# Optimization experiments

Measured on AMD Instinct MI355X. Metric: run time of the kernel, lower is better.

The kernel has to match this reference:

```python
import jax, jax.numpy as jnp
import numpy as np

B, T, H, W, C = 2, 8, 20, 36, 512
NH = 4
HD = C // NH
WS = (5, 9)
EXP = (2, 4)              # window_size // 2
KP = (5, 9)               # focal unfold kernel for level k=0
PADP = (2, 4)
T2T_K, T2T_S, T2T_P = (7, 7), (3, 3), (3, 3)
FFN_HD = 1960
NWH, NWW = H // WS[0], W // WS[1]   # 4, 4
WAREA = WS[0] * WS[1]               # 45


def _valid_ind_rolled():
    wh, ww = WS
    eh, ew = EXP
    m = np.ones((4, wh, ww), np.float32)
    m[0, :wh - eh, :ww - ew] = 0   # tl
    m[1, :wh - eh, ew:] = 0        # tr
    m[2, eh:, :ww - ew] = 0        # bl
    m[3, eh:, ew:] = 0             # br
    return jnp.asarray(np.nonzero(m.reshape(-1))[0])

VALID_ROLLED = _valid_ind_rolled()  # (120,)


def unfold(x, k, s, p):
    # x: (N, Cc, Hh, Ww) -> (N, Cc*kh*kw, L); matches torch.nn.Unfold layout (c slowest).
    N, Cc, Hh, Ww = x.shape
    kh, kw = k; sh, sw = s; ph, pw = p
    xp = jnp.pad(x, ((0, 0), (0, 0), (ph, ph), (pw, pw)))
    oh = (Hh + 2 * ph - kh) // sh + 1
    ow = (Ww + 2 * pw - kw) // sw + 1
    cols = [xp[:, :, i:i + oh * sh:sh, j:j + ow * sw:sw]
            for i in range(kh) for j in range(kw)]
    patches = jnp.stack(cols, axis=2)            # (N, Cc, kh*kw, oh, ow)
    return patches.reshape(N, Cc * kh * kw, oh * ow)


def fold(patches, out_hw, k, s, p):
    # inverse of unfold (overlap-add), matches torch F.fold.
    N = patches.shape[0]
    kh, kw = k; sh, sw = s; ph, pw = p
    Hh, Ww = out_hw
    oh = (Hh + 2 * ph - kh) // sh + 1
    ow = (Ww + 2 * pw - kw) // sw + 1
    Cc = patches.shape[1] // (kh * kw)
    pr = patches.reshape(N, Cc, kh, kw, oh, ow)
    out = jnp.zeros((N, Cc, Hh + 2 * ph, Ww + 2 * pw), patches.dtype)
    for i in range(kh):
        for j in range(kw):
            out = out.at[:, :, i:i + oh * sh:sh, j:j + ow * sw:sw].add(pr[:, :, i, j])
    return out[:, :, ph:ph + Hh, pw:pw + Ww]


def layer_norm(x, g, b):
    mu = jnp.mean(x, -1, keepdims=True)
    var = jnp.var(x, -1, keepdims=True)
    return (x - mu) * jax.lax.rsqrt(var + 1e-5) * g + b


def win_part(x):
    # (B,T,H,W,C) -> (B*nW, T*wh*ww, C)
    b = x.shape[0]
    x = x.reshape(b, T, NWH, WS[0], NWW, WS[1], C)
    return x.transpose(0, 2, 4, 1, 3, 5, 6).reshape(-1, T * WAREA, C)


def to_heads(w):
    return w.reshape(-1, T, WAREA, NH, HD).transpose(0, 3, 1, 2, 4).reshape(-1, NH, T * WAREA, HD)


def block_forward(x, g1, be1, wqkv, bqkv, wproj, bproj, wpool, bpool, g2, be2, w1, bf1, w2, bf2, out_h, out_w):
    shortcut = x
    xn = layer_norm(x, g1, be1)

    # ---- coarser (pooled) focal level, k=0 (focal_level=2) ----
    wnr = xn.reshape(B, T, NWH, WS[0], NWW, WS[1], C).transpose(0, 2, 4, 1, 3, 5, 6)
    wnr = wnr.reshape(B, NWH, NWW, T, WAREA, C)
    pooled = jnp.einsum('bhwtnc,n->bhwtc', wnr, wpool) + bpool   # (B,NWH,NWW,T,C)

    # ---- window attention ----
    qkv = xn @ wqkv + bqkv                                       # (B,T,H,W,3C)
    q, k, v = jnp.split(qkv, 3, axis=-1)
    qw = to_heads(win_part(q)) * (HD ** -0.5)
    kw_, vw = to_heads(win_part(k)), to_heads(win_part(v))

    def rolled(t):
        parts = []
        for sh, sw in ((-EXP[0], -EXP[1]), (-EXP[0], EXP[1]), (EXP[0], -EXP[1]), (EXP[0], EXP[1])):
            r = jnp.roll(t, (sh, sw), axis=(2, 3))
            parts.append(win_part(r).reshape(-1, T, WAREA, NH, HD))
        cat = jnp.concatenate(parts, axis=2)                     # (B*nW, T, 4*warea, NH, HD)
        cat = jnp.take(cat.transpose(0, 3, 1, 2, 4), VALID_ROLLED, axis=3)
        return cat.reshape(-1, NH, T * VALID_ROLLED.shape[0], HD)

    k_rolled = jnp.concatenate([kw_, rolled(k)], axis=2)         # (B*nW, NH, T*165, HD)
    v_rolled = jnp.concatenate([vw, rolled(v)], axis=2)

    # pooled keys/values via focal unfold
    xp = pooled.transpose(0, 3, 1, 2, 4)                          # (B,T,NWH,NWW,C)
    qkv_p = xp @ wqkv + bqkv
    kp, vp = qkv_p[..., C:2 * C], qkv_p[..., 2 * C:]

    def unfold_kv(t):
        t = t.transpose(0, 1, 4, 2, 3).reshape(B * T, C, NWH, NWW)
        u = unfold(t, KP, (1, 1), PADP)                           # (B*T, C*45, L)
        L = u.shape[-1]
        u = u.reshape(B, T, C, KP[0], KP[1], L).transpose(0, 5, 1, 3, 4, 2)
        u = u.reshape(B * L, T, KP[0] * KP[1], NH, HD).transpose(0, 3, 1, 2, 4)
        return u.reshape(B * L, NH, T * KP[0] * KP[1], HD)

    k_all = jnp.concatenate([k_rolled, unfold_kv(kp)], axis=2)
    v_all = jnp.concatenate([v_rolled, unfold_kv(vp)], axis=2)

    attn = jnp.einsum('wnqd,wnkd->wnqk', qw, k_all)               # (B*nW, NH, T*45, N)

    # validity mask for pooled context (zero-padded unfold positions -> -100)
    ones = jnp.ones((T, 1, NWH, NWW), x.dtype)
    um = unfold(ones, KP, (1, 1), PADP)                           # (T, 45, L)
    L = um.shape[-1]
    mvals = jnp.where(um.reshape(T, KP[0] * KP[1], L).transpose(2, 0, 1).reshape(L, -1) == 0,
                      jnp.asarray(-100.0, x.dtype), jnp.asarray(0.0, x.dtype))
    n_rolled = k_rolled.shape[2]
    mask_cols = jnp.concatenate([jnp.zeros((L, n_rolled), x.dtype), mvals], axis=1)
    attn = attn + jnp.tile(mask_cols, (B, 1))[:, None, None, :]

    attn = jax.nn.softmax(attn, axis=-1)
    out = jnp.einsum('wnqk,wnkd->wnqd', attn, v_all)
    out = out.transpose(0, 2, 1, 3).reshape(-1, T * WAREA, C) @ wproj + bproj

    # window reverse + residual
    out = out.reshape(B, NWH, NWW, T, WS[0], WS[1], C)
    out = out.transpose(0, 3, 1, 4, 2, 5, 6).reshape(B, T, H, W, C)
    x = shortcut + out

    # ---- FusionFeedForward (fold/unfold re-normalized MLP) ----
    y = layer_norm(x, g2, be2).reshape(B, T * H * W, C)
    h = y @ w1 + bf1                                              # (B, n, 1960)
    nvec = ((out_h + 2 * T2T_P[0] - T2T_K[0]) // T2T_S[0] + 1) * \
           ((out_w + 2 * T2T_P[1] - T2T_K[1]) // T2T_S[1] + 1)
    bt = (B * T * H * W) // nvec
    norm_p = jnp.ones((bt, T2T_K[0] * T2T_K[1], nvec), x.dtype)
    norm_f = fold(norm_p, (out_h, out_w), T2T_K, T2T_S, T2T_P)    # (bt,1,out_h,out_w)
    h_f = fold(h.reshape(bt, nvec, FFN_HD).transpose(0, 2, 1), (out_h, out_w), T2T_K, T2T_S, T2T_P)
    h = unfold(h_f / norm_f, T2T_K, T2T_S, T2T_P).transpose(0, 2, 1).reshape(B, T * H * W, FFN_HD)
    h = jax.nn.gelu(h, approximate=False) @ w2 + bf2
    return x + h.reshape(B, T, H, W, C)


def setup_inputs() -> dict:
    key = jax.random.key(0)
    ks = jax.random.split(key, 8)
    s = 0.02
    return dict(
        x=jax.random.normal(ks[0], (B, T, H, W, C), jnp.float32),
        g1=jnp.ones((C,), jnp.float32),
        be1=jnp.zeros((C,), jnp.float32),
        wqkv=jax.random.normal(ks[1], (C, 3 * C), jnp.float32) * s,
        bqkv=jnp.zeros((3 * C,), jnp.float32),
        wproj=jax.random.normal(ks[2], (C, C), jnp.float32) * s,
        bproj=jnp.zeros((C,), jnp.float32),
        wpool=jnp.full((WAREA,), 1.0 / WAREA, jnp.float32),
        bpool=jnp.zeros((1,), jnp.float32),
        g2=jnp.ones((C,), jnp.float32),
        be2=jnp.zeros((C,), jnp.float32),
        w1=jax.random.normal(ks[3], (C, FFN_HD), jnp.float32) * s,
        bf1=jnp.zeros((FFN_HD,), jnp.float32),
        w2=jax.random.normal(ks[4], (FFN_HD, C), jnp.float32) * s,
        bf2=jnp.zeros((C,), jnp.float32),
        out_h=60,
        out_w=108,
    )


def reference(x, g1, be1, wqkv, bqkv, wproj, bproj, wpool, bpool, g2, be2, w1, bf1, w2, bf2, out_h, out_w):
    return block_forward(x, g1, be1, wqkv, bqkv, wproj, bproj, wpool, bpool,
                         g2, be2, w1, bf1, w2, bf2, out_h, out_w)
```

## Files before the change

### kernel.cpp

```cpp
#include <hip/hip_runtime.h>
#include <hip/hip_bf16.h>
#include <math.h>

typedef __hip_bfloat16 bf16;
typedef __attribute__((ext_vector_type(8))) short bf16x8;
typedef __attribute__((ext_vector_type(4))) float f32x4;

#define DEVI __device__ __forceinline__

#define C_ 512
#define NH_ 4
#define NTOK 11520
#define NKEY 1680
#define NRK 120
#define FFN_ 1960
#define POOLED_FLAG 0x40000000

DEVI float bfu(unsigned u) { return __uint_as_float(u << 16); }
DEVI float ldf(const bf16* p) { return __bfloat162float(*p); }
DEVI float ldf(const float* p) { return *p; }
DEVI void stw(bf16* p, float v) { *p = __float2bfloat16(v); }
DEVI void stw(float* p, float v) { *p = v; }
DEVI unsigned short f2bs(float f) { bf16 h = __float2bfloat16(f); return *(unsigned short*)&h; }
DEVI unsigned pk2(float a, float b) {
  return (unsigned)f2bs(a) | ((unsigned)f2bs(b) << 16);
}

template <int DT> DEVI float ldw(const void* p, size_t i) {
  if (DT == 0) return __bfloat162float(((const bf16*)p)[i]);
  else         return ((const float*)p)[i];
}

DEVI void gload_lds16(const void* g, void* l) {
  __builtin_amdgcn_global_load_lds(
      (const __attribute__((address_space(1))) void*)g,
      (__attribute__((address_space(3))) void*)l, 16, 0, 0);
}

__global__ void k_detect(const void* __restrict__ g1, int* __restrict__ flag) {
  if (threadIdx.x == 0) {
    const unsigned short* p = (const unsigned short*)g1;
    *flag = (p[0] == 0x3F80u) ? 0 : 1;
  }
}

__global__ void k_prep(int* __restrict__ table) {
  if (threadIdx.x == 0) {
    int cnt = 0;
    for (int p = 0; p < 4; p++)
      for (int wi = 0; wi < 5; wi++)
        for (int wj = 0; wj < 9; wj++) {
          bool invalid;
          if (p == 0)      invalid = (wi < 3) && (wj < 5);
          else if (p == 1) invalid = (wi < 3) && (wj >= 4);
          else if (p == 2) invalid = (wi >= 2) && (wj < 5);
          else             invalid = (wi >= 2) && (wj >= 4);
          if (!invalid) table[cnt++] = p * 45 + wi * 9 + wj;
        }
  }
}

__global__ void k_ksrc(const int* __restrict__ vtab, int* __restrict__ ksrc) {
  int idx = blockIdx.x * 256 + threadIdx.x;
  if (idx >= 32 * NKEY) return;
  int w = idx / NKEY, j = idx % NKEY;
  int b = w >> 4, nh = (w >> 2) & 3, nw = w & 3;
  int val;
  if (j < 360) {
    int t = j / 45, pos = j % 45, wi = pos / 9, wj2 = pos % 9;
    val = ((b * 8 + t) * 20 + nh * 5 + wi) * 36 + nw * 9 + wj2;
  } else if (j < 1320) {
    int jj = j - 360;
    int t = jj / 120, r = jj % 120;
    int id = vtab[r];
    int p = id / 45, pos = id % 45, wi = pos / 9, wj2 = pos % 9;
    int sh = (p < 2) ? -2 : 2;
    int sw = (p & 1) ? 4 : -4;
    int hh = nh * 5 + wi - sh;
    if (hh < 0) hh += 20; else if (hh >= 20) hh -= 20;
    int ww2 = nw * 9 + wj2 - sw;
    if (ww2 < 0) ww2 += 36; else if (ww2 >= 36) ww2 -= 36;
    val = ((b * 8 + t) * 20 + hh) * 36 + ww2;
  } else {
    int jj = j - 1320;
    int t = jj / 45, kidx = jj % 45, ki = kidx / 9, kj = kidx % 9;
    int snh = nh + ki - 2, snw = nw + kj - 4;
    if (snh < 0 || snh >= 4 || snw < 0 || snw >= 4) val = -1;
    else val = POOLED_FLAG | ((b * 8 + t) * 16 + snh * 4 + snw);
  }
  ksrc[idx] = val;
}

template <int DT>
__global__ void k_wcvt(const int* __restrict__ dflag, const void* __restrict__ in,
                       bf16* __restrict__ out, int K, int N, int Npad) {
  if (*dflag != DT) return;
  int idx = blockIdx.x * 256 + threadIdx.x;
  if (idx >= Npad * K) return;
  int n = idx / K, k = idx % K;
  float v = (n < N) ? ldw<DT>(in, (size_t)k * N + n) : 0.f;
  out[idx] = __float2bfloat16(v);
}

template <int DT>
__global__ void k_bcvt(const int* __restrict__ dflag, const void* __restrict__ in,
                       float* __restrict__ out, int n) {
  if (*dflag != DT) return;
  int i = blockIdx.x * 256 + threadIdx.x;
  if (i < n) out[i] = ldw<DT>(in, i);
}

template <int DT, typename InT>
__global__ void k_ln(const int* __restrict__ dflag, const InT* __restrict__ xin,
                     const void* __restrict__ g, const void* __restrict__ be,
                     bf16* __restrict__ out) {
  if (*dflag != DT) return;
  const int tok = blockIdx.x;
  const int tid = threadIdx.x;
  const size_t base = (size_t)tok * C_;
  float v0 = ldf(xin + base + tid);
  float v1 = ldf(xin + base + tid + 256);
  float s = v0 + v1, ss = v0 * v0 + v1 * v1;
#pragma unroll
  for (int o = 32; o; o >>= 1) { s += __shfl_xor(s, o); ss += __shfl_xor(ss, o); }
  __shared__ float sh[10];
  const int lane = tid & 63, wv = tid >> 6;
  if (lane == 0) { sh[wv] = s; sh[4 + wv] = ss; }
  __syncthreads();
  if (tid == 0) {
    float a = sh[0] + sh[1] + sh[2] + sh[3];
    float q = sh[4] + sh[5] + sh[6] + sh[7];
    float mu = a * (1.0f / C_);
    float var = q * (1.0f / C_) - mu * mu;
    sh[8] = mu; sh[9] = rsqrtf(fmaxf(var, 0.f) + 1e-5f);
  }
  __syncthreads();
  float mu = sh[8], inv = sh[9];
  stw(out + base + tid,
      (v0 - mu) * inv * ldw<DT>(g, tid) + ldw<DT>(be, tid));
  stw(out + base + tid + 256,
      (v1 - mu) * inv * ldw<DT>(g, tid + 256) + ldw<DT>(be, tid + 256));
}

template <int DT>
__global__ void k_pool(const int* __restrict__ dflag, const bf16* __restrict__ xn,
                       const void* __restrict__ wpool, const void* __restrict__ bpool,
                       float* __restrict__ pooled) {
  if (*dflag != DT) return;
  int idx = blockIdx.x * blockDim.x + threadIdx.x;
  if (idx >= 256 * C_) return;
  int c = idx & (C_ - 1);
  int fw = idx >> 9;
  int nw = fw & 3, nh = (fw >> 2) & 3;
  int bt = fw >> 4;
  float acc = ldw<DT>(bpool, 0);
  for (int wi = 0; wi < 5; wi++) {
    int hh = nh * 5 + wi;
    const bf16* base = xn + (((size_t)(bt * 20 + hh)) * 36 + nw * 9) * C_ + c;
    for (int wj = 0; wj < 9; wj++)
      acc += __bfloat162float(base[(size_t)wj * C_]) * ldw<DT>(wpool, wi * 9 + wj);
  }
  pooled[idx] = acc;
}

template <int DT>
__global__ void k_gemm_small(const int* __restrict__ dflag, const float* __restrict__ A,
                             const void* __restrict__ Bw, const void* __restrict__ bias,
                             float* __restrict__ Cc) {
  if (*dflag != DT) return;
  int n = blockIdx.x * blockDim.x + threadIdx.x;
  int m = blockIdx.y;
  if (n >= 1536) return;
  float acc = ldw<DT>(bias, n);
  const float* a = A + (size_t)m * C_;
  for (int k = 0; k < C_; k++)
    acc += a[k] * ldw<DT>(Bw, (size_t)k * 1536 + n);
  Cc[(size_t)m * 1536 + n] = acc;
}

template <int DT, int RES, typename OutT>
__global__ __launch_bounds__(256) void k_gemm_m(const int* __restrict__ dflag,
                                                const bf16* __restrict__ A,
                                                const bf16* __restrict__ Bt,
                                                const float* __restrict__ bias,
                                                const void* __restrict__ resid,
                                                OutT* __restrict__ out,
                                                int M, int N, int K) {
  if (dflag && *dflag != DT) return;
  __shared__ __align__(16) unsigned short As[128 * 32];
  __shared__ __align__(16) unsigned short Bs[128 * 32];
  const int tid = threadIdx.x;
  const int lane = tid & 63, wid = tid >> 6;
  const int r15 = lane & 15, quad = lane >> 4;
  const int wm = wid >> 1, wn = wid & 1;
  const int m0 = blockIdx.y * 128, n0 = blockIdx.x * 128;

  f32x4 acc[4][4];
#pragma unroll
  for (int i = 0; i < 4; i++)
#pragma unroll
    for (int j = 0; j < 4; j++)
#pragma unroll
      for (int e = 0; e < 4; e++) acc[i][j][e] = 0.f;

  const int lrow = lane >> 2, lcol = (lane & 3) * 8;

  for (int k0 = 0; k0 < K; k0 += 32) {
    int rem = K - k0;
    if (rem >= 32) {
      const bf16* ga = A + (size_t)(m0 + wid * 32 + lrow) * K + k0 + lcol;
      gload_lds16(ga, &As[wid * 1024]);
      gload_lds16(ga + (size_t)16 * K, &As[wid * 1024 + 512]);
      const bf16* gb = Bt + (size_t)(n0 + wid * 32 + lrow) * K + k0 + lcol;
      gload_lds16(gb, &Bs[wid * 1024]);
      gload_lds16(gb + (size_t)16 * K, &Bs[wid * 1024 + 512]);
    } else {
      int r = tid >> 2, c = (tid & 3) * 8;
      uint4 z = make_uint4(0, 0, 0, 0);
      uint4 a0 = z, a1 = z, b0 = z, b1 = z;
      if (c < rem) {
        a0 = *(const uint4*)(A + (size_t)(m0 + r) * K + k0 + c);
        a1 = *(const uint4*)(A + (size_t)(m0 + r + 64) * K + k0 + c);
        b0 = *(const uint4*)(Bt + (size_t)(n0 + r) * K + k0 + c);
        b1 = *(const uint4*)(Bt + (size_t)(n0 + r + 64) * K + k0 + c);
      }
      *(uint4*)&As[r * 32 + c] = a0;
      *(uint4*)&As[(r + 64) * 32 + c] = a1;
      *(uint4*)&Bs[r * 32 + c] = b0;
      *(uint4*)&Bs[(r + 64) * 32 + c] = b1;
    }
    __syncthreads();

    bf16x8 af[4], bfr[4];
#pragma unroll
    for (int mf = 0; mf < 4; mf++)
      af[mf] = *(const bf16x8*)&As[(wm * 64 + mf * 16 + r15) * 32 + quad * 8];
#pragma unroll
    for (int nf = 0; nf < 4; nf++)
      bfr[nf] = *(const bf16x8*)&Bs[(wn * 64 + nf * 16 + r15) * 32 + quad * 8];
#pragma unroll
    for (int mf = 0; mf < 4; mf++)
#pragma unroll
      for (int nf = 0; nf < 4; nf++)
        acc[mf][nf] = __builtin_amdgcn_mfma_f32_16x16x32_bf16(af[mf], bfr[nf],
                                                              acc[mf][nf], 0, 0, 0);
    __syncthreads();
  }

#pragma unroll
  for (int nf = 0; nf < 4; nf++) {
    int n = n0 + wn * 64 + nf * 16 + r15;
    if (n >= N) continue;
    float bv = bias[n];
#pragma unroll
    for (int mf = 0; mf < 4; mf++) {
      int mb = m0 + wm * 64 + mf * 16 + quad * 4;
#pragma unroll
      for (int e = 0; e < 4; e++) {
        size_t off = (size_t)(mb + e) * N + n;
        float v = acc[mf][nf][e] + bv;
        if (RES == 1) v += ldw<DT>(resid, off);
        else if (RES == 2) v += ((const float*)resid)[off];
        stw(out + off, v);
      }
    }
  }
}

#define KT 64
#define KPAD 136
#define VPAD 72
__global__ __launch_bounds__(256) void k_attn_m(const bf16* __restrict__ qkv,
                                                const float* __restrict__ qkvp,
                                                const int* __restrict__ ksrc,
                                                bf16* __restrict__ ao) {
  __shared__ int ks_l[NKEY];
  __shared__ __align__(16) unsigned short ktl[KT * KPAD];
  __shared__ __align__(16) unsigned short vtl[128 * VPAD];
  __shared__ __align__(16) unsigned short ptl[4 * 16 * VPAD];
  __shared__ float maskv[KT];

  const int tid = threadIdx.x;
  const int lane = tid & 63, wid = tid >> 6;
  const int r15 = lane & 15, quad = lane >> 4;
  const int qt = blockIdx.x, n = blockIdx.y, w = blockIdx.z;
  const int b = w >> 4, nh = (w >> 2) & 3, nw = w & 3;
  const unsigned short* qkvs = (const unsigned short*)qkv;

  for (int j = tid; j < NKEY; j += 256) ks_l[j] = ksrc[w * NKEY + j];

  bf16x8 qf[4];
  {
    int qw = qt * 64 + wid * 16 + r15;
    int qc2 = qw < 360 ? qw : 359;
    int t = qc2 / 45, pos = qc2 % 45, wi = pos / 9, wj = pos % 9;
    int tok = ((b * 8 + t) * 20 + nh * 5 + wi) * 36 + nw * 9 + wj;
    const unsigned short* qp = qkvs + (size_t)tok * 1536 + n * 128 + quad * 8;
#pragma unroll
    for (int c = 0; c < 4; c++)
      qf[c] = *(const bf16x8*)(qp + c * 32);
  }

  f32x4 of[8];
#pragma unroll
  for (int nt = 0; nt < 8; nt++)
#pragma unroll
    for (int e = 0; e < 4; e++) of[nt][e] = 0.f;
  float m_[4], l_[4];
#pragma unroll
  for (int e = 0; e < 4; e++) { m_[e] = -1e30f; l_[e] = 0.f; }

  unsigned short* ptw = &ptl[wid * 16 * VPAD];
  __syncthreads();

  for (int j0 = 0; j0 < NKEY; j0 += KT) {
    const int cnt = (NKEY - j0) < KT ? (NKEY - j0) : KT;
    {
      const int r = tid >> 2, p = tid & 3;
      int s0 = (r < cnt) ? ks_l[j0 + r] : -1;
      if (p == 0) maskv[r] = (s0 < 0) ? -30000.f : 0.f;
      unsigned short* krow = &ktl[r * KPAD + p * 32];
      if (s0 < 0) {
        uint4 z = make_uint4(0, 0, 0, 0);
#pragma unroll
        for (int i = 0; i < 4; i++) *(uint4*)(krow + i * 8) = z;
#pragma unroll
        for (int i = 0; i < 32; i++) vtl[(p * 32 + i) * VPAD + r] = 0;
      } else if (s0 & POOLED_FLAG) {
        int tp = s0 & 0x3FFFFFFF;
        const float* kf = qkvp + (size_t)tp * 1536 + 512 + n * 128 + p * 32;
        const float* vf = kf + 512;
#pragma unroll
        for (int i = 0; i < 4; i++) {
          float4 f0 = ((const float4*)kf)[2 * i], f1 = ((const float4*)kf)[2 * i + 1];
          *(uint4*)(krow + i * 8) =
              make_uint4(pk2(f0.x, f0.y), pk2(f0.z, f0.w), pk2(f1.x, f1.y), pk2(f1.z, f1.w));
          float4 g0 = ((const float4*)vf)[2 * i], g1 = ((const float4*)vf)[2 * i + 1];
          int d0 = p * 32 + i * 8;
          vtl[(d0 + 0) * VPAD + r] = f2bs(g0.x);
          vtl[(d0 + 1) * VPAD + r] = f2bs(g0.y);
          vtl[(d0 + 2) * VPAD + r] = f2bs(g0.z);
          vtl[(d0 + 3) * VPAD + r] = f2bs(g0.w);
          vtl[(d0 + 4) * VPAD + r] = f2bs(g1.x);
          vtl[(d0 + 5) * VPAD + r] = f2bs(g1.y);
          vtl[(d0 + 6) * VPAD + r] = f2bs(g1.z);
          vtl[(d0 + 7) * VPAD + r] = f2bs(g1.w);
        }
      } else {
        const unsigned short* kq = qkvs + (size_t)s0 * 1536 + 512 + n * 128 + p * 32;
#pragma unroll
        for (int i = 0; i < 4; i++) *(uint4*)(krow + i * 8) = ((const uint4*)kq)[i];
        const unsigned short* vq = kq + 512;
#pragma unroll
        for (int i = 0; i < 4; i++) {
          uint4 u = ((const uint4*)vq)[i];
          int d0 = p * 32 + i * 8;
          vtl[(d0 + 0) * VPAD + r] = (unsigned short)(u.x & 0xFFFFu);
          vtl[(d0 + 1) * VPAD + r] = (unsigned short)(u.x >> 16);
          vtl[(d0 + 2) * VPAD + r] = (unsigned short)(u.y & 0xFFFFu);
          vtl[(d0 + 3) * VPAD + r] = (unsigned short)(u.y >> 16);
          vtl[(d0 + 4) * VPAD + r] = (unsigned short)(u.z & 0xFFFFu);
          vtl[(d0 + 5) * VPAD + r] = (unsigned short)(u.z >> 16);
          vtl[(d0 + 6) * VPAD + r] = (unsigned short)(u.w & 0xFFFFu);
          vtl[(d0 + 7) * VPAD + r] = (unsigned short)(u.w >> 16);
        }
      }
    }
    __syncthreads();

    f32x4 sf[4];
#pragma unroll
    for (int ft = 0; ft < 4; ft++)
#pragma unroll
      for (int e = 0; e < 4; e++) sf[ft][e] = 0.f;
#pragma unroll
    for (int kc = 0; kc < 4; kc++) {
      bf16x8 a = qf[kc];
#pragma unroll
      for (int ft = 0; ft < 4; ft++) {
        bf16x8 bb = *(const bf16x8*)&ktl[(ft * 16 + r15) * KPAD + kc * 32 + quad * 8];
        sf[ft] = __builtin_amdgcn_mfma_f32_16x16x32_bf16(a, bb, sf[ft], 0, 0, 0);
      }
    }
    const float scl = 0.088388347648318447f;
#pragma unroll
    for (int ft = 0; ft < 4; ft++) {
      float mk = maskv[ft * 16 + r15];
#pragma unroll
      for (int e = 0; e < 4; e++) sf[ft][e] = sf[ft][e] * scl + mk;
    }
    float tm[4], rs[4];
#pragma unroll
    for (int e = 0; e < 4; e++) {
      float v = fmaxf(fmaxf(sf[0][e], sf[1][e]), fmaxf(sf[2][e], sf[3][e]));
#pragma unroll
      for (int o = 1; o < 16; o <<= 1) v = fmaxf(v, __shfl_xor(v, o));
      tm[e] = v;
    }
#pragma unroll
    for (int e = 0; e < 4; e++) {
      float mn = fmaxf(m_[e], tm[e]);
      float alpha = __expf(m_[e] - mn);
      m_[e] = mn;
      rs[e] = 0.f;
#pragma unroll
      for (int ft = 0; ft < 4; ft++) {
        float pv = __expf(sf[ft][e] - mn);
        rs[e] += pv;
        ptw[(quad * 4 + e) * VPAD + ft * 16 + r15] = f2bs(pv);
      }
#pragma unroll
      for (int o = 1; o < 16; o <<= 1) rs[e] += __shfl_xor(rs[e], o);
      l_[e] = l_[e] * alpha + rs[e];
#pragma unroll
      for (int nt = 0; nt < 8; nt++) of[nt][e] *= alpha;
    }
#pragma unroll
    for (int kc = 0; kc < 2; kc++) {
      bf16x8 pa = *(const bf16x8*)&ptw[r15 * VPAD + kc * 32 + quad * 8];
#pragma unroll
      for (int nt = 0; nt < 8; nt++) {
        bf16x8 vb = *(const bf16x8*)&vtl[(nt * 16 + r15) * VPAD + kc * 32 + quad * 8];
        of[nt] = __builtin_amdgcn_mfma_f32_16x16x32_bf16(pa, vb, of[nt], 0, 0, 0);
      }
    }
    __syncthreads();
  }

#pragma unroll
  for (int e = 0; e < 4; e++) {
    int qw = qt * 64 + wid * 16 + quad * 4 + e;
    if (qw >= 360) continue;
    float inv = 1.0f / l_[e];
    int t = qw / 45, pos = qw % 45, wi = pos / 9, wj = pos % 9;
    int tok = ((b * 8 + t) * 20 + nh * 5 + wi) * 36 + nw * 9 + wj;
    bf16* op = ao + (size_t)tok * 512 + n * 128 + r15;
#pragma unroll
    for (int nt = 0; nt < 8; nt++)
      stw(op + nt * 16, of[nt][e] * inv);
  }
}

__global__ void k_fold(const bf16* __restrict__ h1, float* __restrict__ hf) {
  int idx = blockIdx.x * 256 + threadIdx.x;
  if (idx >= 16 * 40 * 60 * 108) return;
  int x = idx % 108;
  int tmp = idx / 108;
  int y = tmp % 60; tmp /= 60;
  int c = tmp % 40;
  int bt = tmp / 40;
  float sum = 0.f;
  int cnt = 0;
  for (int ki = y % 3; ki < 7; ki += 3) {
    int num = y + 3 - ki;
    if (num < 0) continue;
    int oh = num / 3;
    if (oh >= 20) continue;
    for (int kj = x % 3; kj < 7; kj += 3) {
      int num2 = x + 3 - kj;
      if (num2 < 0) continue;
      int ow = num2 / 3;
      if (ow >= 36) continue;
      sum += __bfloat162float(
          h1[(size_t)(bt * 720 + oh * 36 + ow) * FFN_ + c * 49 + ki * 7 + kj]);
      cnt++;
    }
  }
  hf[idx] = sum / (float)cnt;
}

__global__ void k_unfold_gelu(const float* __restrict__ hf, bf16* __restrict__ h2) {
  int idx = blockIdx.x * 256 + threadIdx.x;
  if (idx >= NTOK * FFN_) return;
  int f = idx % FFN_;
  int token = idx / FFN_;
  int c = f / 49, k = f % 49, ki = k / 7, kj = k % 7;
  int bt = token / 720, vec = token % 720;
  int oh = vec / 36, ow = vec % 36;
  int y = oh * 3 + ki - 3, x = ow * 3 + kj - 3;
  float v = 0.f;
  if (y >= 0 && y < 60 && x >= 0 && x < 108)
    v = hf[((size_t)(bt * 40 + c) * 60 + y) * 108 + x];
  float g = 0.5f * v * (1.0f + erff(v * 0.70710678118654752f));
  stw(h2 + idx, g);
}

extern "C" void kernel_launch(void* const* d_in, const int* in_sizes, int n_in,
                              void* d_out, int out_size, void* d_ws, size_t ws_size,
                              hipStream_t stream) {
  (void)in_sizes; (void)n_in; (void)out_size; (void)ws_size;
  const void* x     = d_in[0];
  const void* g1    = d_in[1];
  const void* be1   = d_in[2];
  const void* wqkv  = d_in[3];
  const void* bqkv  = d_in[4];
  const void* wproj = d_in[5];
  const void* bproj = d_in[6];
  const void* wpool = d_in[7];
  const void* bpool = d_in[8];
  const void* g2    = d_in[9];
  const void* be2   = d_in[10];
  const void* w1    = d_in[11];
  const void* bf1   = d_in[12];
  const void* w2    = d_in[13];
  const void* bf2   = d_in[14];

  char* ws = (char*)d_ws;
  size_t off = 0;
  auto alloc = [&](size_t bytes) -> void* {
    void* p = ws + off;
    off += (bytes + 255) & ~(size_t)255;
    return p;
  };

  int*   dflag  = (int*)  alloc(256);
  int*   vtab   = (int*)  alloc(NRK * sizeof(int));
  int*   ksrc   = (int*)  alloc((size_t)32 * NKEY * sizeof(int));
  bf16*  buf2   = (bf16*) alloc((size_t)NTOK * FFN_ * 2);
  float* pooled = (float*)alloc((size_t)256 * C_ * 4);
  float* qkvp   = (float*)alloc((size_t)256 * 1536 * 4);
  float* x2     = (float*)alloc((size_t)NTOK * C_ * 4);
  float* hf     = (float*)alloc((size_t)16 * 40 * 60 * 108 * 4);
  bf16*  wqkv_t = (bf16*) alloc((size_t)1536 * 512 * 2);
  bf16*  wproj_t= (bf16*) alloc((size_t)512 * 512 * 2);
  bf16*  w1_t   = (bf16*) alloc((size_t)2048 * 512 * 2);
  bf16*  w2_t   = (bf16*) alloc((size_t)512 * FFN_ * 2);
  float* bqkv_f = (float*)alloc(1536 * 4);
  float* bproj_f= (float*)alloc(512 * 4);
  float* bf1_f  = (float*)alloc(FFN_ * 4);
  float* bf2_f  = (float*)alloc(512 * 4);

  bf16* buf1 = (bf16*)d_out;
  bf16* xn = buf1;
  bf16* ao = buf1;
  bf16* y  = buf1;
  bf16* qkv = buf2;
  bf16* h1  = buf2;

  k_detect<<<1, 64, 0, stream>>>(g1, dflag);
  k_prep<<<1, 64, 0, stream>>>(vtab);
  k_ksrc<<<(32 * NKEY) / 256, 256, 0, stream>>>(vtab, ksrc);

  k_wcvt<0><<<(1536 * 512) / 256, 256, 0, stream>>>(dflag, wqkv, wqkv_t, 512, 1536, 1536);
  k_wcvt<1><<<(1536 * 512) / 256, 256, 0, stream>>>(dflag, wqkv, wqkv_t, 512, 1536, 1536);
  k_wcvt<0><<<(512 * 512) / 256, 256, 0, stream>>>(dflag, wproj, wproj_t, 512, 512, 512);
  k_wcvt<1><<<(512 * 512) / 256, 256, 0, stream>>>(dflag, wproj, wproj_t, 512, 512, 512);
  k_wcvt<0><<<(2048 * 512) / 256, 256, 0, stream>>>(dflag, w1, w1_t, 512, FFN_, 2048);
  k_wcvt<1><<<(2048 * 512) / 256, 256, 0, stream>>>(dflag, w1, w1_t, 512, FFN_, 2048);
  k_wcvt<0><<<(512 * FFN_ + 255) / 256, 256, 0, stream>>>(dflag, w2, w2_t, FFN_, 512, 512);
  k_wcvt<1><<<(512 * FFN_ + 255) / 256, 256, 0, stream>>>(dflag, w2, w2_t, FFN_, 512, 512);
  k_bcvt<0><<<6, 256, 0, stream>>>(dflag, bqkv, bqkv_f, 1536);
  k_bcvt<1><<<6, 256, 0, stream>>>(dflag, bqkv, bqkv_f, 1536);
  k_bcvt<0><<<2, 256, 0, stream>>>(dflag, bproj, bproj_f, 512);
  k_bcvt<1><<<2, 256, 0, stream>>>(dflag, bproj, bproj_f, 512);
  k_bcvt<0><<<8, 256, 0, stream>>>(dflag, bf1, bf1_f, FFN_);
  k_bcvt<1><<<8, 256, 0, stream>>>(dflag, bf1, bf1_f, FFN_);
  k_bcvt<0><<<2, 256, 0, stream>>>(dflag, bf2, bf2_f, 512);
  k_bcvt<1><<<2, 256, 0, stream>>>(dflag, bf2, bf2_f, 512);

  k_ln<0, bf16><<<NTOK, 256, 0, stream>>>(dflag, (const bf16*)x, g1, be1, xn);
  k_ln<1, float><<<NTOK, 256, 0, stream>>>(dflag, (const float*)x, g1, be1, xn);

  k_pool<0><<<512, 256, 0, stream>>>(dflag, xn, wpool, bpool, pooled);
  k_pool<1><<<512, 256, 0, stream>>>(dflag, xn, wpool, bpool, pooled);

  k_gemm_m<0, 0, bf16><<<dim3(12, 90), 256, 0, stream>>>(
      nullptr, xn, wqkv_t, bqkv_f, nullptr, qkv, NTOK, 1536, 512);

  k_gemm_small<0><<<dim3(6, 256), 256, 0, stream>>>(dflag, pooled, wqkv, bqkv, qkvp);
  k_gemm_small<1><<<dim3(6, 256), 256, 0, stream>>>(dflag, pooled, wqkv, bqkv, qkvp);

  k_attn_m<<<dim3(6, NH_, 32), 256, 0, stream>>>(qkv, qkvp, ksrc, ao);

  k_gemm_m<0, 1, float><<<dim3(4, 90), 256, 0, stream>>>(
      dflag, ao, wproj_t, bproj_f, x, x2, NTOK, 512, 512);
  k_gemm_m<1, 1, float><<<dim3(4, 90), 256, 0, stream>>>(
      dflag, ao, wproj_t, bproj_f, x, x2, NTOK, 512, 512);

  k_ln<0, float><<<NTOK, 256, 0, stream>>>(dflag, x2, g2, be2, y);
  k_ln<1, float><<<NTOK, 256, 0, stream>>>(dflag, x2, g2, be2, y);

  k_gemm_m<0, 0, bf16><<<dim3(16, 90), 256, 0, stream>>>(
      nullptr, y, w1_t, bf1_f, nullptr, h1, NTOK, FFN_, 512);

  k_fold<<<(16 * 40 * 60 * 108) / 256, 256, 0, stream>>>(h1, hf);

  k_unfold_gelu<<<(NTOK * FFN_) / 256, 256, 0, stream>>>(hf, h1);

  k_gemm_m<0, 2, bf16><<<dim3(4, 90), 256, 0, stream>>>(
      dflag, h1, w2_t, bf2_f, x2, (bf16*)d_out, NTOK, 512, FFN_);
  k_gemm_m<1, 2, float><<<dim3(4, 90), 256, 0, stream>>>(
      dflag, h1, w2_t, bf2_f, x2, (float*)d_out, NTOK, 512, FFN_);
}
```

Baseline: 655.9 us.

## Prefetch next K/V tile into registers during attention compute and reorder grid

The attention kernel now loads the next 64-key tile of K and V into registers while the MFMA work on the current tile runs, then writes it to shared memory between two barriers. The goal is to hide gather latency behind compute instead of stalling before each tile. The V gather now has each thread handle one key row across a quarter of the head dim, so per-thread transposed stores are spread more evenly. The grid is also reordered so that adjacent blocks cover different windows, which changes how blocks are scheduled and how cache is reused. The register cost of holding the prefetched tile (32 extra VGPRs) may lower occupancy.

```diff
diff --git a/kernel.cpp b/kernel.cpp
--- a/kernel.cpp
+++ b/kernel.cpp
@@ -283,7 +283,7 @@
   const int tid = threadIdx.x;
   const int lane = tid & 63, wid = tid >> 6;
   const int r15 = lane & 15, quad = lane >> 4;
-  const int qt = blockIdx.x, n = blockIdx.y, w = blockIdx.z;
+  const int w = blockIdx.x, qt = blockIdx.y, n = blockIdx.z;
   const int b = w >> 4, nh = (w >> 2) & 3, nw = w & 3;
   const unsigned short* qkvs = (const unsigned short*)qkv;
 
@@ -313,60 +313,80 @@
   unsigned short* ptw = &ptl[wid * 16 * VPAD];
   __syncthreads();
 
-  for (int j0 = 0; j0 < NKEY; j0 += KT) {
-    const int cnt = (NKEY - j0) < KT ? (NKEY - j0) : KT;
+  const int kr = tid >> 2, kp = tid & 3;
+  const int vr = lane, vp = wid;
+  uint4 kreg[4], vreg[4];
+  float mreg = -30000.f;
+
+  auto load_tile = [&](int j0) {
+    int cnt = NKEY - j0; if (cnt > KT) cnt = KT;
     {
-      const int r = tid >> 2, p = tid & 3;
-      int s0 = (r < cnt) ? ks_l[j0 + r] : -1;
-      if (p == 0) maskv[r] = (s0 < 0) ? -30000.f : 0.f;
-      unsigned short* krow = &ktl[r * KPAD + p * 32];
+      int s0 = (kr < cnt) ? ks_l[j0 + kr] : -1;
+      mreg = (s0 < 0) ? -30000.f : 0.f;
       if (s0 < 0) {
-        uint4 z = make_uint4(0, 0, 0, 0);
-#pragma unroll
-        for (int i = 0; i < 4; i++) *(uint4*)(krow + i * 8) = z;
-#pragma unroll
-        for (int i = 0; i < 32; i++) vtl[(p * 32 + i) * VPAD + r] = 0;
+        kreg[0] = kreg[1] = kreg[2] = kreg[3] = make_uint4(0, 0, 0, 0);
       } else if (s0 & POOLED_FLAG) {
-        int tp = s0 & 0x3FFFFFFF;
-        const float* kf = qkvp + (size_t)tp * 1536 + 512 + n * 128 + p * 32;
-        const float* vf = kf + 512;
+        const float* kf = qkvp + (size_t)(s0 & 0x3FFFFFFF) * 1536 + 512 + n * 128 + kp * 32;
 #pragma unroll
         for (int i = 0; i < 4; i++) {
           float4 f0 = ((const float4*)kf)[2 * i], f1 = ((const float4*)kf)[2 * i + 1];
-          *(uint4*)(krow + i * 8) =
-              make_uint4(pk2(f0.x, f0.y), pk2(f0.z, f0.w), pk2(f1.x, f1.y), pk2(f1.z, f1.w));
-          float4 g0 = ((const float4*)vf)[2 * i], g1 = ((const float4*)vf)[2 * i + 1];
-          int d0 = p * 32 + i * 8;
-          vtl[(d0 + 0) * VPAD + r] = f2bs(g0.x);
-          vtl[(d0 + 1) * VPAD + r] = f2bs(g0.y);
-          vtl[(d0 + 2) * VPAD + r] = f2bs(g0.z);
-          vtl[(d0 + 3) * VPAD + r] = f2bs(g0.w);
-          vtl[(d0 + 4) * VPAD + r] = f2bs(g1.x);
-          vtl[(d0 + 5) * VPAD + r] = f2bs(g1.y);
-          vtl[(d0 + 6) * VPAD + r] = f2bs(g1.z);
-          vtl[(d0 + 7) * VPAD + r] = f2bs(g1.w);
+          kreg[i] = make_uint4(pk2(f0.x, f0.y), pk2(f0.z, f0.w),
+                               pk2(f1.x, f1.y), pk2(f1.z, f1.w));
         }
       } else {
-        const unsigned short* kq = qkvs + (size_t)s0 * 1536 + 512 + n * 128 + p * 32;
-#pragma unroll
-        for (int i = 0; i < 4; i++) *(uint4*)(krow + i * 8) = ((const uint4*)kq)[i];
-        const unsigned short* vq = kq + 512;
+        const uint4* kq = (const uint4*)(qkvs + (size_t)s0 * 1536 + 512 + n * 128 + kp * 32);
+#pragma unroll
+        for (int i = 0; i < 4; i++) kreg[i] = kq[i];
+      }
+    }
+    {
+      int s1 = (vr < cnt) ? ks_l[j0 + vr] : -1;
+      if (s1 < 0) {
+        vreg[0] = vreg[1] = vreg[2] = vreg[3] = make_uint4(0, 0, 0, 0);
+      } else if (s1 & POOLED_FLAG) {
+        const float* vf = qkvp + (size_t)(s1 & 0x3FFFFFFF) * 1536 + 1024 + n * 128 + vp * 32;
 #pragma unroll
         for (int i = 0; i < 4; i++) {
-          uint4 u = ((const uint4*)vq)[i];
-          int d0 = p * 32 + i * 8;
-          vtl[(d0 + 0) * VPAD + r] = (unsigned short)(u.x & 0xFFFFu);
-          vtl[(d0 + 1) * VPAD + r] = (unsigned short)(u.x >> 16);
-          vtl[(d0 + 2) * VPAD + r] = (unsigned short)(u.y & 0xFFFFu);
-          vtl[(d0 + 3) * VPAD + r] = (unsigned short)(u.y >> 16);
-          vtl[(d0 + 4) * VPAD + r] = (unsigned short)(u.z & 0xFFFFu);
-          vtl[(d0 + 5) * VPAD + r] = (unsigned short)(u.z >> 16);
-          vtl[(d0 + 6) * VPAD + r] = (unsigned short)(u.w & 0xFFFFu);
-          vtl[(d0 + 7) * VPAD + r] = (unsigned short)(u.w >> 16);
+          float4 f0 = ((const float4*)vf)[2 * i], f1 = ((const float4*)vf)[2 * i + 1];
+          vreg[i] = make_uint4(pk2(f0.x, f0.y), pk2(f0.z, f0.w),
+                               pk2(f1.x, f1.y), pk2(f1.z, f1.w));
         }
+      } else {
+        const uint4* vq = (const uint4*)(qkvs + (size_t)s1 * 1536 + 1024 + n * 128 + vp * 32);
+#pragma unroll
+        for (int i = 0; i < 4; i++) vreg[i] = vq[i];
       }
     }
-    __syncthreads();
+  };
+
+  auto store_tile = [&]() {
+    if (kp == 0) maskv[kr] = mreg;
+#pragma unroll
+    for (int i = 0; i < 4; i++)
+      *(uint4*)&ktl[kr * KPAD + kp * 32 + i * 8] = kreg[i];
+#pragma unroll
+    for (int i = 0; i < 4; i++) {
+      uint4 u = vreg[i];
+      int d0 = vp * 32 + i * 8;
+      vtl[(d0 + 0) * VPAD + vr] = (unsigned short)(u.x & 0xFFFFu);
+      vtl[(d0 + 1) * VPAD + vr] = (unsigned short)(u.x >> 16);
+      vtl[(d0 + 2) * VPAD + vr] = (unsigned short)(u.y & 0xFFFFu);
+      vtl[(d0 + 3) * VPAD + vr] = (unsigned short)(u.y >> 16);
+      vtl[(d0 + 4) * VPAD + vr] = (unsigned short)(u.z & 0xFFFFu);
+      vtl[(d0 + 5) * VPAD + vr] = (unsigned short)(u.z >> 16);
+      vtl[(d0 + 6) * VPAD + vr] = (unsigned short)(u.w & 0xFFFFu);
+      vtl[(d0 + 7) * VPAD + vr] = (unsigned short)(u.w >> 16);
+    }
+  };
+
+  load_tile(0);
+  store_tile();
+  __syncthreads();
+
+  int j0 = 0;
+  while (true) {
+    int nxt = j0 + KT;
+    if (nxt < NKEY) load_tile(nxt);
 
     f32x4 sf[4];
 #pragma unroll
@@ -424,7 +444,12 @@
         of[nt] = __builtin_amdgcn_mfma_f32_16x16x32_bf16(pa, vb, of[nt], 0, 0, 0);
       }
     }
+
+    if (nxt >= NKEY) break;
     __syncthreads();
+    store_tile();
+    __syncthreads();
+    j0 = nxt;
   }
 
 #pragma unroll
@@ -570,7 +595,7 @@
   k_gemm_small<0><<<dim3(6, 256), 256, 0, stream>>>(dflag, pooled, wqkv, bqkv, qkvp);
   k_gemm_small<1><<<dim3(6, 256), 256, 0, stream>>>(dflag, pooled, wqkv, bqkv, qkvp);
 
-  k_attn_m<<<dim3(6, NH_, 32), 256, 0, stream>>>(qkv, qkvp, ksrc, ao);
+  k_attn_m<<<dim3(32, 6, NH_), 256, 0, stream>>>(qkv, qkvp, ksrc, ao);
 
   k_gemm_m<0, 1, float><<<dim3(4, 90), 256, 0, stream>>>(
       dflag, ao, wproj_t, bproj_f, x, x2, NTOK, 512, 512);
```

Result: faster. 636.4 us (-3.0%).
